# Optimization experiments

Hardware: AMD Instinct MI355X
Metric: run time of the kernel (lower is better)

The kernel has to match this reference:

```python
import jax, jax.numpy as jnp
import numpy as np

N_NODES = 100000
N_EDGES = 800000
IN_DIM = 128
HIDDEN_DIM = 256
OUT_DIM = 40


def setup_inputs() -> dict:
    key = jax.random.key(0)
    k_x, k_e, k_w1, k_w2 = jax.random.split(key, 4)
    x = jax.random.normal(k_x, (N_NODES, IN_DIM), dtype=jnp.float32)
    edge_index = jax.random.randint(k_e, (2, N_EDGES), 0, N_NODES, dtype=jnp.int32)
    # Glorot-style init like PyG GCNConv
    s1 = 1.0 / np.sqrt(IN_DIM)
    s2 = 1.0 / np.sqrt(HIDDEN_DIM)
    W1 = jax.random.uniform(k_w1, (IN_DIM, HIDDEN_DIM), dtype=jnp.float32, minval=-s1, maxval=s1)
    b1 = jnp.zeros((HIDDEN_DIM,), dtype=jnp.float32)
    W2 = jax.random.uniform(k_w2, (HIDDEN_DIM, OUT_DIM), dtype=jnp.float32, minval=-s2, maxval=s2)
    b2 = jnp.zeros((OUT_DIM,), dtype=jnp.float32)
    return {"x": x, "edge_index": edge_index, "W1": W1, "b1": b1, "W2": W2, "b2": b2}


def _gcn_conv(x, W, b, src, dst, n_nodes):
    # PyG GCNConv: linear transform, add self-loops, symmetric normalization,
    # scatter-add aggregation, then bias.
    h = x @ W  # [N, F_out]
    loops = jnp.arange(n_nodes, dtype=src.dtype)
    s = jnp.concatenate([src, loops])  # [E+N]
    d = jnp.concatenate([dst, loops])
    deg = jax.ops.segment_sum(jnp.ones_like(d, dtype=h.dtype), d, num_segments=n_nodes)
    dinv = jax.lax.rsqrt(jnp.maximum(deg, 1.0))  # deg >= 1 with self-loops
    norm = dinv[s] * dinv[d]  # [E+N]
    msgs = h[s] * norm[:, None]  # [E+N, F_out] -- dominant memory traffic
    out = jax.ops.segment_sum(msgs, d, num_segments=n_nodes)
    return out + b


def reference(x, edge_index, W1, b1, W2, b2):
    src, dst = edge_index[0], edge_index[1]
    n = x.shape[0]
    h = _gcn_conv(x, W1, b1, src, dst, n)
    h = jax.nn.relu(h)
    # dropout is identity in eval mode
    h = _gcn_conv(h, W2, b2, src, dst, n)
    return jax.nn.log_softmax(h, axis=1)
```

## Files before the change

### kernel.cpp

```cpp
#include <hip/hip_runtime.h>
#include <math.h>

#define N_NODES 100000
#define N_EDGES 800000
#define IN_DIM 128
#define HIDDEN_DIM 256
#define OUT_DIM 40
#define CAP 32
#define SHARD_DIV 12500
#define NPAIRS (N_NODES * 64)
#define T1 (HIDDEN_DIM * IN_DIM)
#define T2 (64 * HIDDEN_DIM)

typedef __attribute__((ext_vector_type(8))) __bf16 bf16x8;
typedef __attribute__((ext_vector_type(4))) float f32x4;

#define FIXSC 131072.0f
#define FIXSC_INV 7.62939453125e-6f

__device__ __forceinline__ unsigned short f2bf(float f) {
    unsigned u = __float_as_uint(f);
    unsigned r = (u + 0x7FFFu + ((u >> 16) & 1u)) >> 16;
    return (unsigned short)r;
}
__device__ __forceinline__ float bflo(unsigned v) { return __uint_as_float(v << 16); }
__device__ __forceinline__ float bfhi(unsigned v) { return __uint_as_float(v & 0xFFFF0000u); }
__device__ __forceinline__ float bfs(unsigned short v) { return __uint_as_float((unsigned)v << 16); }

__device__ __forceinline__ bf16x8 ld_frag16(const unsigned short* p) {
    union { uint4 u; bf16x8 b; } t;
    t.u = *(const uint4*)p;
    return t.b;
}

__global__ __launch_bounds__(256) void fill_kernel(const int* __restrict__ src,
                                                   const int* __restrict__ dst,
                                                   int* __restrict__ cnt,
                                                   int* __restrict__ esrc, int e) {
    int shard = blockIdx.x & 7;
    int i = (blockIdx.x >> 3) * 256 + threadIdx.x;
    if (i < e) {
        int d = dst[i];
        if (d / SHARD_DIV == shard) {
            int p = atomicAdd(&cnt[d], 1);
            if (p < CAP) esrc[d * CAP + p] = src[i];
        }
    }
}

__global__ __launch_bounds__(256) void cast_kernel(const float* __restrict__ x,
                                                   const int* __restrict__ cnt,
                                                   unsigned* __restrict__ xs,
                                                   const float* __restrict__ W1,
                                                   unsigned short* __restrict__ W1t,
                                                   const float* __restrict__ W2,
                                                   unsigned short* __restrict__ W2t) {
    int i = blockIdx.x * 256 + threadIdx.x;
    if (i < NPAIRS) {
        float dn = rsqrtf((float)cnt[i >> 6] + 1.0f) * FIXSC;
        float2 v = ((const float2*)x)[i];
        xs[i] = (unsigned)f2bf(v.x * dn) | ((unsigned)f2bf(v.y * dn) << 16);
    }
    if (i < T1) {
        int n = i >> 7, k = i & 127;
        W1t[i] = f2bf(W1[(size_t)k * HIDDEN_DIM + n]);
    } else if (i < T1 + T2) {
        int j = i - T1;
        int n = j >> 8, k = j & 255;
        float v = (n < OUT_DIM) ? W2[(size_t)k * OUT_DIM + n] : 0.0f;
        W2t[j] = f2bf(v);
    }
}

__global__ __launch_bounds__(256) void aggx_kernel(const unsigned* __restrict__ xs,
                                                   const int* __restrict__ cnt,
                                                   const int* __restrict__ esrc,
                                                   unsigned* __restrict__ aggxb, int n) {
    int wid = (blockIdx.x * 256 + threadIdx.x) >> 6;
    int lane = threadIdx.x & 63;
    if (wid >= n) return;
    int c = cnt[wid];
    int m = c < CAP ? c : CAP;
    unsigned v = xs[(size_t)wid * 64 + lane];
    int ia = (int)bflo(v), ib = (int)bfhi(v);
    int base = wid * CAP;
    int j = 0;
    for (; j + 7 < m; j += 8) {
        int s0 = esrc[base + j],     s1 = esrc[base + j + 1];
        int s2 = esrc[base + j + 2], s3 = esrc[base + j + 3];
        int s4 = esrc[base + j + 4], s5 = esrc[base + j + 5];
        int s6 = esrc[base + j + 6], s7 = esrc[base + j + 7];
        unsigned u0 = xs[(size_t)s0 * 64 + lane];
        unsigned u1 = xs[(size_t)s1 * 64 + lane];
        unsigned u2 = xs[(size_t)s2 * 64 + lane];
        unsigned u3 = xs[(size_t)s3 * 64 + lane];
        unsigned u4 = xs[(size_t)s4 * 64 + lane];
        unsigned u5 = xs[(size_t)s5 * 64 + lane];
        unsigned u6 = xs[(size_t)s6 * 64 + lane];
        unsigned u7 = xs[(size_t)s7 * 64 + lane];
        ia += ((int)bflo(u0) + (int)bflo(u1)) + ((int)bflo(u2) + (int)bflo(u3))
            + ((int)bflo(u4) + (int)bflo(u5)) + ((int)bflo(u6) + (int)bflo(u7));
        ib += ((int)bfhi(u0) + (int)bfhi(u1)) + ((int)bfhi(u2) + (int)bfhi(u3))
            + ((int)bfhi(u4) + (int)bfhi(u5)) + ((int)bfhi(u6) + (int)bfhi(u7));
    }
    for (; j + 3 < m; j += 4) {
        int s0 = esrc[base + j],     s1 = esrc[base + j + 1];
        int s2 = esrc[base + j + 2], s3 = esrc[base + j + 3];
        unsigned u0 = xs[(size_t)s0 * 64 + lane];
        unsigned u1 = xs[(size_t)s1 * 64 + lane];
        unsigned u2 = xs[(size_t)s2 * 64 + lane];
        unsigned u3 = xs[(size_t)s3 * 64 + lane];
        ia += ((int)bflo(u0) + (int)bflo(u1)) + ((int)bflo(u2) + (int)bflo(u3));
        ib += ((int)bfhi(u0) + (int)bfhi(u1)) + ((int)bfhi(u2) + (int)bfhi(u3));
    }
    for (; j < m; j++) {
        unsigned u = xs[(size_t)esrc[base + j] * 64 + lane];
        ia += (int)bflo(u); ib += (int)bfhi(u);
    }
    float k = rsqrtf((float)c + 1.0f) * FIXSC_INV;
    float ax = (float)ia * k, ay = (float)ib * k;
    aggxb[(size_t)wid * 64 + lane] = (unsigned)f2bf(ax) | ((unsigned)f2bf(ay) << 16);
}

#define ASTR 40
template<int KDIM, bool BIAS_RELU, bool SCALE>
__global__ __launch_bounds__(256) void mfma_gemm(const unsigned short* __restrict__ A,
                                                 const unsigned short* __restrict__ Bt,
                                                 unsigned short* __restrict__ C,
                                                 const float* __restrict__ bias,
                                                 const int* __restrict__ cnt,
                                                 int M, int N) {
    __shared__ __align__(16) unsigned short As[128 * ASTR];
    __shared__ __align__(16) unsigned short Bs[64 * ASTR];
    int tid = threadIdx.x;
    int wv = tid >> 6, lane = tid & 63;
    int quad = lane >> 4, l16 = lane & 15;
    int m0 = blockIdx.x * 128;
    int n0 = blockIdx.y * 64;

    f32x4 zero4 = {0.f, 0.f, 0.f, 0.f};
    f32x4 acc[2][4];
#pragma unroll
    for (int rt = 0; rt < 2; rt++)
#pragma unroll
        for (int ct = 0; ct < 4; ct++) acc[rt][ct] = zero4;

    for (int k0 = 0; k0 < KDIM; k0 += 32) {
#pragma unroll
        for (int rep = 0; rep < 2; rep++) {
            int lin = rep * 256 + tid;
            int row = lin >> 2, ch = lin & 3;
            int gm = m0 + row;
            uint4 v = make_uint4(0u, 0u, 0u, 0u);
            if (gm < M) v = *(const uint4*)&A[(size_t)gm * KDIM + k0 + ch * 8];
            *(uint4*)&As[row * ASTR + ch * 8] = v;
        }
        {
            int row = tid >> 2, ch = tid & 3;
            uint4 v = *(const uint4*)&Bt[(size_t)(n0 + row) * KDIM + k0 + ch * 8];
            *(uint4*)&Bs[row * ASTR + ch * 8] = v;
        }
        __syncthreads();

        bf16x8 af[2], bfr[4];
#pragma unroll
        for (int rt = 0; rt < 2; rt++)
            af[rt] = ld_frag16(&As[(wv * 32 + rt * 16 + l16) * ASTR + quad * 8]);
#pragma unroll
        for (int ct = 0; ct < 4; ct++)
            bfr[ct] = ld_frag16(&Bs[(ct * 16 + l16) * ASTR + quad * 8]);
#pragma unroll
        for (int rt = 0; rt < 2; rt++)
#pragma unroll
            for (int ct = 0; ct < 4; ct++)
                acc[rt][ct] = __builtin_amdgcn_mfma_f32_16x16x32_bf16(af[rt], bfr[ct], acc[rt][ct], 0, 0, 0);
        __syncthreads();
    }

#pragma unroll
    for (int rt = 0; rt < 2; rt++) {
#pragma unroll
        for (int ct = 0; ct < 4; ct++) {
            int col = n0 + ct * 16 + l16;
            if (col >= N) continue;
            float bv = BIAS_RELU ? bias[col] : 0.0f;
#pragma unroll
            for (int r = 0; r < 4; r++) {
                int gm = m0 + wv * 32 + rt * 16 + quad * 4 + r;
                if (gm >= M) continue;
                float v = acc[rt][ct][r];
                if (BIAS_RELU) v = fmaxf(v + bv, 0.0f);
                if (SCALE) v *= rsqrtf((float)cnt[gm] + 1.0f) * FIXSC;
                C[(size_t)gm * N + col] = f2bf(v);
            }
        }
    }
}

__global__ __launch_bounds__(256) void agg2_kernel(const unsigned short* __restrict__ h2s,
                                                   const int* __restrict__ cnt,
                                                   const int* __restrict__ esrc,
                                                   const float* __restrict__ b2,
                                                   float* __restrict__ out, int n) {
    int wid = (blockIdx.x * 256 + threadIdx.x) >> 6;
    int lane = threadIdx.x & 63;
    if (wid >= n) return;
    int c = cnt[wid];
    int m = c < CAP ? c : CAP;
    int base = wid * CAP;
    int ia = (int)bfs(h2s[(size_t)wid * 64 + lane]);
    int j = 0;
    for (; j + 7 < m; j += 8) {
        int s0 = esrc[base + j],     s1 = esrc[base + j + 1];
        int s2 = esrc[base + j + 2], s3 = esrc[base + j + 3];
        int s4 = esrc[base + j + 4], s5 = esrc[base + j + 5];
        int s6 = esrc[base + j + 6], s7 = esrc[base + j + 7];
        int v0 = (int)bfs(h2s[(size_t)s0 * 64 + lane]);
        int v1 = (int)bfs(h2s[(size_t)s1 * 64 + lane]);
        int v2 = (int)bfs(h2s[(size_t)s2 * 64 + lane]);
        int v3 = (int)bfs(h2s[(size_t)s3 * 64 + lane]);
        int v4 = (int)bfs(h2s[(size_t)s4 * 64 + lane]);
        int v5 = (int)bfs(h2s[(size_t)s5 * 64 + lane]);
        int v6 = (int)bfs(h2s[(size_t)s6 * 64 + lane]);
        int v7 = (int)bfs(h2s[(size_t)s7 * 64 + lane]);
        ia += ((v0 + v1) + (v2 + v3)) + ((v4 + v5) + (v6 + v7));
    }
    for (; j + 3 < m; j += 4) {
        int s0 = esrc[base + j],     s1 = esrc[base + j + 1];
        int s2 = esrc[base + j + 2], s3 = esrc[base + j + 3];
        int v0 = (int)bfs(h2s[(size_t)s0 * 64 + lane]);
        int v1 = (int)bfs(h2s[(size_t)s1 * 64 + lane]);
        int v2 = (int)bfs(h2s[(size_t)s2 * 64 + lane]);
        int v3 = (int)bfs(h2s[(size_t)s3 * 64 + lane]);
        ia += (v0 + v1) + (v2 + v3);
    }
    for (; j < m; j++) ia += (int)bfs(h2s[(size_t)esrc[base + j] * 64 + lane]);

    float k = rsqrtf((float)c + 1.0f) * FIXSC_INV;
    bool act = (lane < OUT_DIM);
    float v = act ? fmaf((float)ia, k, b2[lane]) : -INFINITY;
    float mx = v;
#pragma unroll
    for (int o = 32; o > 0; o >>= 1) mx = fmaxf(mx, __shfl_xor(mx, o));
    float e = act ? __expf(v - mx) : 0.0f;
    float ssum = e;
#pragma unroll
    for (int o = 32; o > 0; o >>= 1) ssum += __shfl_xor(ssum, o);
    if (act) out[(size_t)wid * OUT_DIM + lane] = v - mx - __logf(ssum);
}

extern "C" void kernel_launch(void* const* d_in, const int* in_sizes, int n_in,
                              void* d_out, int out_size, void* d_ws, size_t ws_size,
                              hipStream_t stream) {
    const float* x  = (const float*)d_in[0];
    const int* ei   = (const int*)d_in[1];
    const float* W1 = (const float*)d_in[2];
    const float* b1 = (const float*)d_in[3];
    const float* W2 = (const float*)d_in[4];
    const float* b2 = (const float*)d_in[5];
    float* out = (float*)d_out;

    const int* src = ei;
    const int* dst = ei + N_EDGES;

    char* ws = (char*)d_ws;
    size_t off = 0;
    auto carve = [&](size_t bytes) -> char* {
        char* p = ws + off;
        off = (off + bytes + 255) & ~(size_t)255;
        return p;
    };
    int*      cnt   = (int*)     carve((size_t)N_NODES * 4);
    int*      esrc  = (int*)     carve((size_t)N_NODES * CAP * 4);
    unsigned* xs    = (unsigned*)carve((size_t)N_NODES * 64 * 4);
    unsigned short* W1t = (unsigned short*)carve((size_t)T1 * 2);
    unsigned short* W2t = (unsigned short*)carve((size_t)T2 * 2);
    unsigned* aggxb = (unsigned*)carve((size_t)N_NODES * 64 * 4);
    unsigned short* h1b = (unsigned short*)carve((size_t)N_NODES * HIDDEN_DIM * 2);
    unsigned short* h2s = (unsigned short*)aggxb;

    hipMemsetAsync(cnt, 0, (size_t)N_NODES * 4, stream);
    fill_kernel<<<((N_EDGES + 255) / 256) * 8, 256, 0, stream>>>(src, dst, cnt, esrc, N_EDGES);
    cast_kernel<<<(NPAIRS + 255) / 256, 256, 0, stream>>>(x, cnt, xs, W1, W1t, W2, W2t);
    aggx_kernel<<<(N_NODES * 64 + 255) / 256, 256, 0, stream>>>(xs, cnt, esrc, aggxb, N_NODES);
    {
        dim3 grid((N_NODES + 127) / 128, HIDDEN_DIM / 64);
        mfma_gemm<IN_DIM, true, false><<<grid, 256, 0, stream>>>(
            (const unsigned short*)aggxb, W1t, h1b, b1, nullptr, N_NODES, HIDDEN_DIM);
    }
    {
        dim3 grid((N_NODES + 127) / 128, 1);
        mfma_gemm<HIDDEN_DIM, false, true><<<grid, 256, 0, stream>>>(
            h1b, W2t, h2s, nullptr, cnt, N_NODES, 64);
    }
    agg2_kernel<<<(N_NODES * 64 + 255) / 256, 256, 0, stream>>>(h2s, cnt, esrc, b2, out, N_NODES);
}
```

Before: 287.2 us.

## Fuse both dense GEMMs into one kernel and pack two features per lane in agg2

Result: faster. 279.2 us (-2.8%).

```diff
diff --git a/kernel.cpp b/kernel.cpp
--- a/kernel.cpp
+++ b/kernel.cpp
@@ -25,7 +25,6 @@
 }
 __device__ __forceinline__ float bflo(unsigned v) { return __uint_as_float(v << 16); }
 __device__ __forceinline__ float bfhi(unsigned v) { return __uint_as_float(v & 0xFFFF0000u); }
-__device__ __forceinline__ float bfs(unsigned short v) { return __uint_as_float((unsigned)v << 16); }
 
 __device__ __forceinline__ bf16x8 ld_frag16(const unsigned short* p) {
     union { uint4 u; bf16x8 b; } t;
@@ -122,131 +121,177 @@
     aggxb[(size_t)wid * 64 + lane] = (unsigned)f2bf(ax) | ((unsigned)f2bf(ay) << 16);
 }
 
-#define ASTR 40
-template<int KDIM, bool BIAS_RELU, bool SCALE>
-__global__ __launch_bounds__(256) void mfma_gemm(const unsigned short* __restrict__ A,
-                                                 const unsigned short* __restrict__ Bt,
-                                                 unsigned short* __restrict__ C,
-                                                 const float* __restrict__ bias,
-                                                 const int* __restrict__ cnt,
-                                                 int M, int N) {
-    __shared__ __align__(16) unsigned short As[128 * ASTR];
-    __shared__ __align__(16) unsigned short Bs[64 * ASTR];
+#define BSTR 40
+#define HSTR 136
+__global__ __launch_bounds__(256) void gemm12_kernel(const unsigned short* __restrict__ A,
+                                                     const unsigned short* __restrict__ W1t,
+                                                     const unsigned short* __restrict__ W2t,
+                                                     const float* __restrict__ b1,
+                                                     const int* __restrict__ cnt,
+                                                     unsigned short* __restrict__ h2s,
+                                                     int M) {
+    __shared__ __align__(16) unsigned short Bs[256 * BSTR];
+    __shared__ __align__(16) unsigned short Hs[4 * 32 * HSTR];
     int tid = threadIdx.x;
     int wv = tid >> 6, lane = tid & 63;
     int quad = lane >> 4, l16 = lane & 15;
     int m0 = blockIdx.x * 128;
-    int n0 = blockIdx.y * 64;
+
+    float bv[16];
+#pragma unroll
+    for (int ct = 0; ct < 16; ct++) bv[ct] = b1[ct * 16 + l16];
 
     f32x4 zero4 = {0.f, 0.f, 0.f, 0.f};
-    f32x4 acc[2][4];
+    f32x4 acc[2][16];
 #pragma unroll
     for (int rt = 0; rt < 2; rt++)
 #pragma unroll
-        for (int ct = 0; ct < 4; ct++) acc[rt][ct] = zero4;
-
-    for (int k0 = 0; k0 < KDIM; k0 += 32) {
-#pragma unroll
-        for (int rep = 0; rep < 2; rep++) {
+        for (int ct = 0; ct < 16; ct++) acc[rt][ct] = zero4;
+
+    for (int k0 = 0; k0 < 128; k0 += 32) {
+#pragma unroll
+        for (int rep = 0; rep < 4; rep++) {
             int lin = rep * 256 + tid;
             int row = lin >> 2, ch = lin & 3;
-            int gm = m0 + row;
-            uint4 v = make_uint4(0u, 0u, 0u, 0u);
-            if (gm < M) v = *(const uint4*)&A[(size_t)gm * KDIM + k0 + ch * 8];
-            *(uint4*)&As[row * ASTR + ch * 8] = v;
-        }
-        {
-            int row = tid >> 2, ch = tid & 3;
-            uint4 v = *(const uint4*)&Bt[(size_t)(n0 + row) * KDIM + k0 + ch * 8];
-            *(uint4*)&Bs[row * ASTR + ch * 8] = v;
+            *(uint4*)&Bs[row * BSTR + ch * 8] =
+                *(const uint4*)&W1t[(size_t)row * 128 + k0 + ch * 8];
         }
         __syncthreads();
-
-        bf16x8 af[2], bfr[4];
+        bf16x8 af[2];
+#pragma unroll
+        for (int rt = 0; rt < 2; rt++) {
+            int gm = m0 + wv * 32 + rt * 16 + l16;
+            union { uint4 u; bf16x8 b; } cv;
+            cv.u = make_uint4(0u, 0u, 0u, 0u);
+            if (gm < M) cv.u = *(const uint4*)&A[(size_t)gm * 128 + k0 + quad * 8];
+            af[rt] = cv.b;
+        }
+#pragma unroll
+        for (int ct = 0; ct < 16; ct++) {
+            bf16x8 bfr = ld_frag16(&Bs[(ct * 16 + l16) * BSTR + quad * 8]);
+#pragma unroll
+            for (int rt = 0; rt < 2; rt++)
+                acc[rt][ct] = __builtin_amdgcn_mfma_f32_16x16x32_bf16(af[rt], bfr, acc[rt][ct], 0, 0, 0);
+        }
+        __syncthreads();
+    }
+
+    unsigned short* hw = &Hs[wv * 32 * HSTR];
+    f32x4 acc2[2][4];
+#pragma unroll
+    for (int rt = 0; rt < 2; rt++)
+#pragma unroll
+        for (int c2 = 0; c2 < 4; c2++) acc2[rt][c2] = zero4;
+
+#pragma unroll
+    for (int chunk = 0; chunk < 2; chunk++) {
 #pragma unroll
         for (int rt = 0; rt < 2; rt++)
-            af[rt] = ld_frag16(&As[(wv * 32 + rt * 16 + l16) * ASTR + quad * 8]);
-#pragma unroll
-        for (int ct = 0; ct < 4; ct++)
-            bfr[ct] = ld_frag16(&Bs[(ct * 16 + l16) * ASTR + quad * 8]);
-#pragma unroll
-        for (int rt = 0; rt < 2; rt++)
-#pragma unroll
-            for (int ct = 0; ct < 4; ct++)
-                acc[rt][ct] = __builtin_amdgcn_mfma_f32_16x16x32_bf16(af[rt], bfr[ct], acc[rt][ct], 0, 0, 0);
-        __syncthreads();
-    }
-
-#pragma unroll
-    for (int rt = 0; rt < 2; rt++) {
-#pragma unroll
-        for (int ct = 0; ct < 4; ct++) {
-            int col = n0 + ct * 16 + l16;
-            if (col >= N) continue;
-            float bv = BIAS_RELU ? bias[col] : 0.0f;
+#pragma unroll
+            for (int c8 = 0; c8 < 8; c8++) {
+                int ct = chunk * 8 + c8;
+#pragma unroll
+                for (int r = 0; r < 4; r++) {
+                    int row = rt * 16 + quad * 4 + r;
+                    float v = fmaxf(acc[rt][ct][r] + bv[ct], 0.0f);
+                    hw[row * HSTR + c8 * 16 + l16] = f2bf(v);
+                }
+            }
+#pragma unroll
+        for (int kk = 0; kk < 4; kk++) {
+            bf16x8 af2[2];
+#pragma unroll
+            for (int rt = 0; rt < 2; rt++)
+                af2[rt] = ld_frag16(&hw[(rt * 16 + l16) * HSTR + kk * 32 + quad * 8]);
+#pragma unroll
+            for (int c2 = 0; c2 < 4; c2++) {
+                bf16x8 bfr = ld_frag16(&W2t[(size_t)(c2 * 16 + l16) * 256 + chunk * 128 + kk * 32 + quad * 8]);
+#pragma unroll
+                for (int rt = 0; rt < 2; rt++)
+                    acc2[rt][c2] = __builtin_amdgcn_mfma_f32_16x16x32_bf16(af2[rt], bfr, acc2[rt][c2], 0, 0, 0);
+            }
+        }
+    }
+
+#pragma unroll
+    for (int rt = 0; rt < 2; rt++)
+#pragma unroll
+        for (int c2 = 0; c2 < 4; c2++) {
+            int col = c2 * 16 + l16;
 #pragma unroll
             for (int r = 0; r < 4; r++) {
                 int gm = m0 + wv * 32 + rt * 16 + quad * 4 + r;
-                if (gm >= M) continue;
-                float v = acc[rt][ct][r];
-                if (BIAS_RELU) v = fmaxf(v + bv, 0.0f);
-                if (SCALE) v *= rsqrtf((float)cnt[gm] + 1.0f) * FIXSC;
-                C[(size_t)gm * N + col] = f2bf(v);
+                if (gm < M) {
+                    float v = acc2[rt][c2][r] * (rsqrtf((float)cnt[gm] + 1.0f) * FIXSC);
+                    h2s[(size_t)gm * 64 + col] = f2bf(v);
+                }
             }
         }
-    }
-}
-
-__global__ __launch_bounds__(256) void agg2_kernel(const unsigned short* __restrict__ h2s,
+}
+
+__global__ __launch_bounds__(256) void agg2_kernel(const unsigned* __restrict__ h2u,
                                                    const int* __restrict__ cnt,
                                                    const int* __restrict__ esrc,
                                                    const float* __restrict__ b2,
                                                    float* __restrict__ out, int n) {
-    int wid = (blockIdx.x * 256 + threadIdx.x) >> 6;
+    int wave = (blockIdx.x * 256 + threadIdx.x) >> 6;
     int lane = threadIdx.x & 63;
-    if (wid >= n) return;
-    int c = cnt[wid];
+    int half = lane >> 5, l32 = lane & 31;
+    int node = wave * 2 + half;
+    if (node >= n) return;
+    int c = cnt[node];
     int m = c < CAP ? c : CAP;
-    int base = wid * CAP;
-    int ia = (int)bfs(h2s[(size_t)wid * 64 + lane]);
+    int base = node * CAP;
+    unsigned v = h2u[(size_t)node * 32 + l32];
+    int ia = (int)bflo(v), ib = (int)bfhi(v);
     int j = 0;
     for (; j + 7 < m; j += 8) {
         int s0 = esrc[base + j],     s1 = esrc[base + j + 1];
         int s2 = esrc[base + j + 2], s3 = esrc[base + j + 3];
         int s4 = esrc[base + j + 4], s5 = esrc[base + j + 5];
         int s6 = esrc[base + j + 6], s7 = esrc[base + j + 7];
-        int v0 = (int)bfs(h2s[(size_t)s0 * 64 + lane]);
-        int v1 = (int)bfs(h2s[(size_t)s1 * 64 + lane]);
-        int v2 = (int)bfs(h2s[(size_t)s2 * 64 + lane]);
-        int v3 = (int)bfs(h2s[(size_t)s3 * 64 + lane]);
-        int v4 = (int)bfs(h2s[(size_t)s4 * 64 + lane]);
-        int v5 = (int)bfs(h2s[(size_t)s5 * 64 + lane]);
-        int v6 = (int)bfs(h2s[(size_t)s6 * 64 + lane]);
-        int v7 = (int)bfs(h2s[(size_t)s7 * 64 + lane]);
-        ia += ((v0 + v1) + (v2 + v3)) + ((v4 + v5) + (v6 + v7));
+        unsigned u0 = h2u[(size_t)s0 * 32 + l32];
+        unsigned u1 = h2u[(size_t)s1 * 32 + l32];
+        unsigned u2 = h2u[(size_t)s2 * 32 + l32];
+        unsigned u3 = h2u[(size_t)s3 * 32 + l32];
+        unsigned u4 = h2u[(size_t)s4 * 32 + l32];
+        unsigned u5 = h2u[(size_t)s5 * 32 + l32];
+        unsigned u6 = h2u[(size_t)s6 * 32 + l32];
+        unsigned u7 = h2u[(size_t)s7 * 32 + l32];
+        ia += ((int)bflo(u0) + (int)bflo(u1)) + ((int)bflo(u2) + (int)bflo(u3))
+            + ((int)bflo(u4) + (int)bflo(u5)) + ((int)bflo(u6) + (int)bflo(u7));
+        ib += ((int)bfhi(u0) + (int)bfhi(u1)) + ((int)bfhi(u2) + (int)bfhi(u3))
+            + ((int)bfhi(u4) + (int)bfhi(u5)) + ((int)bfhi(u6) + (int)bfhi(u7));
     }
     for (; j + 3 < m; j += 4) {
         int s0 = esrc[base + j],     s1 = esrc[base + j + 1];
         int s2 = esrc[base + j + 2], s3 = esrc[base + j + 3];
-        int v0 = (int)bfs(h2s[(size_t)s0 * 64 + lane]);
-        int v1 = (int)bfs(h2s[(size_t)s1 * 64 + lane]);
-        int v2 = (int)bfs(h2s[(size_t)s2 * 64 + lane]);
-        int v3 = (int)bfs(h2s[(size_t)s3 * 64 + lane]);
-        ia += (v0 + v1) + (v2 + v3);
-    }
-    for (; j < m; j++) ia += (int)bfs(h2s[(size_t)esrc[base + j] * 64 + lane]);
-
+        unsigned u0 = h2u[(size_t)s0 * 32 + l32];
+        unsigned u1 = h2u[(size_t)s1 * 32 + l32];
+        unsigned u2 = h2u[(size_t)s2 * 32 + l32];
+        unsigned u3 = h2u[(size_t)s3 * 32 + l32];
+        ia += ((int)bflo(u0) + (int)bflo(u1)) + ((int)bflo(u2) + (int)bflo(u3));
+        ib += ((int)bfhi(u0) + (int)bfhi(u1)) + ((int)bfhi(u2) + (int)bfhi(u3));
+    }
+    for (; j < m; j++) {
+        unsigned u = h2u[(size_t)esrc[base + j] * 32 + l32];
+        ia += (int)bflo(u); ib += (int)bfhi(u);
+    }
     float k = rsqrtf((float)c + 1.0f) * FIXSC_INV;
-    bool act = (lane < OUT_DIM);
-    float v = act ? fmaf((float)ia, k, b2[lane]) : -INFINITY;
-    float mx = v;
-#pragma unroll
-    for (int o = 32; o > 0; o >>= 1) mx = fmaxf(mx, __shfl_xor(mx, o));
-    float e = act ? __expf(v - mx) : 0.0f;
-    float ssum = e;
-#pragma unroll
-    for (int o = 32; o > 0; o >>= 1) ssum += __shfl_xor(ssum, o);
-    if (act) out[(size_t)wid * OUT_DIM + lane] = v - mx - __logf(ssum);
+    int f0 = 2 * l32;
+    bool a0 = (f0 < OUT_DIM), a1 = (f0 + 1 < OUT_DIM);
+    float v0 = a0 ? fmaf((float)ia, k, b2[f0]) : -INFINITY;
+    float v1 = a1 ? fmaf((float)ib, k, b2[f0 + 1]) : -INFINITY;
+    float mx = fmaxf(v0, v1);
+#pragma unroll
+    for (int o = 16; o > 0; o >>= 1) mx = fmaxf(mx, __shfl_xor(mx, o));
+    float e = (a0 ? __expf(v0 - mx) : 0.0f) + (a1 ? __expf(v1 - mx) : 0.0f);
+#pragma unroll
+    for (int o = 16; o > 0; o >>= 1) e += __shfl_xor(e, o);
+    if (a0) {
+        float ls = __logf(e);
+        *(float2*)&out[(size_t)node * OUT_DIM + f0] = make_float2(v0 - mx - ls, v1 - mx - ls);
+    }
 }
 
 extern "C" void kernel_launch(void* const* d_in, const int* in_sizes, int n_in,
@@ -276,22 +321,14 @@
     unsigned short* W1t = (unsigned short*)carve((size_t)T1 * 2);
     unsigned short* W2t = (unsigned short*)carve((size_t)T2 * 2);
     unsigned* aggxb = (unsigned*)carve((size_t)N_NODES * 64 * 4);
-    unsigned short* h1b = (unsigned short*)carve((size_t)N_NODES * HIDDEN_DIM * 2);
-    unsigned short* h2s = (unsigned short*)aggxb;
+    unsigned short* h2s = (unsigned short*)carve((size_t)N_NODES * 64 * 2);
 
     hipMemsetAsync(cnt, 0, (size_t)N_NODES * 4, stream);
     fill_kernel<<<((N_EDGES + 255) / 256) * 8, 256, 0, stream>>>(src, dst, cnt, esrc, N_EDGES);
     cast_kernel<<<(NPAIRS + 255) / 256, 256, 0, stream>>>(x, cnt, xs, W1, W1t, W2, W2t);
     aggx_kernel<<<(N_NODES * 64 + 255) / 256, 256, 0, stream>>>(xs, cnt, esrc, aggxb, N_NODES);
-    {
-        dim3 grid((N_NODES + 127) / 128, HIDDEN_DIM / 64);
-        mfma_gemm<IN_DIM, true, false><<<grid, 256, 0, stream>>>(
-            (const unsigned short*)aggxb, W1t, h1b, b1, nullptr, N_NODES, HIDDEN_DIM);
-    }
-    {
-        dim3 grid((N_NODES + 127) / 128, 1);
-        mfma_gemm<HIDDEN_DIM, false, true><<<grid, 256, 0, stream>>>(
-            h1b, W2t, h2s, nullptr, cnt, N_NODES, 64);
-    }
-    agg2_kernel<<<(N_NODES * 64 + 255) / 256, 256, 0, stream>>>(h2s, cnt, esrc, b2, out, N_NODES);
-}
+    gemm12_kernel<<<(N_NODES + 127) / 128, 256, 0, stream>>>(
+        (const unsigned short*)aggxb, W1t, W2t, b1, cnt, h2s, N_NODES);
+    agg2_kernel<<<((N_NODES + 1) / 2 * 64 + 255) / 256, 256, 0, stream>>>(
+        (const unsigned*)h2s, cnt, esrc, b2, out, N_NODES);
+}
```
